# Performance work log

Measured on AMD Instinct MI355X. Metric: run time of the kernel, lower is better.

Reference implementation:

```python
import jax, jax.numpy as jnp
import numpy as np

B, T, D, H = 2, 2048, 1024, 16
DH = D // H
SCALE = DH ** -0.5
NEG_INF = float(np.finfo(np.float32).min)


def setup_inputs() -> dict:
    key = jax.random.key(0)
    ks = jax.random.split(key, 8)
    query = jax.random.normal(ks[0], (B, T, D), dtype=jnp.float32)
    key_t = jax.random.normal(ks[1], (B, T, D), dtype=jnp.float32)
    value = jax.random.normal(ks[2], (B, T, D), dtype=jnp.float32)
    # causal mask: True means blocked (upper triangle)
    mask = ~jnp.tril(jnp.ones((T, T), dtype=bool))
    # key padding: pad tail beyond a random valid length per batch row
    lens = jax.random.randint(ks[3], (B,), T // 2, T)
    key_padding_mask = jnp.arange(T)[None, :] >= lens[:, None]  # [B, T] True = pad
    s = D ** -0.5
    Wq = jax.random.normal(ks[4], (D, D), dtype=jnp.float32) * s
    Wk = jax.random.normal(ks[5], (D, D), dtype=jnp.float32) * s
    Wv = jax.random.normal(ks[6], (D, D), dtype=jnp.float32) * s
    Wo = jax.random.normal(ks[7], (D, D), dtype=jnp.float32) * s
    return {"query": query, "key": key_t, "value": value, "mask": mask,
            "key_padding_mask": key_padding_mask, "Wq": Wq, "Wk": Wk, "Wv": Wv, "Wo": Wo}


def reference(query, key, value, mask, key_padding_mask, Wq, Wk, Wv, Wo):
    # Linear (no bias): y = x @ W.T, then split heads -> [B, H, T, DH]
    def proj(x, W, Tlen):
        return jnp.einsum('btd,ed->bte', x, W).reshape(B, Tlen, H, DH).transpose(0, 2, 1, 3)

    q = proj(query, Wq, T)
    k = proj(key, Wk, T)
    v = proj(value, Wv, T)

    attn = jnp.einsum('bhqd,bhkd->bhqk', q, k) * SCALE  # [B, H, Tq, Tk]
    attn = jnp.where(mask[None, None, :, :], -jnp.inf, attn)
    attn = jnp.where(key_padding_mask[:, None, None, :], -jnp.inf, attn)
    # rows of batches where ALL keys are padding: zero the logits (softmax -> uniform)
    all_masked = jnp.all(key_padding_mask, axis=-1)[:, None, None, None]
    attn = jnp.where(all_masked, 0.0, attn)

    p = jax.nn.softmax(attn, axis=-1)
    p = jnp.where(jnp.isnan(p), 0.0, p)  # scrub NaN rows (all -inf)

    out = jnp.einsum('bhqk,bhkd->bhqd', p, v)
    out = out.transpose(0, 2, 1, 3).reshape(B, T, D)
    return jnp.einsum('btd,ed->bte', out, Wo)
```

## Files before the change

### kernel.cpp

```cpp
#include <hip/hip_runtime.h>

#define B_  2
#define T_  2048
#define D_  1024
#define H_  16
#define DH_ 64
#define M_  4096

typedef _Float16 f16;
typedef _Float16 f16x8 __attribute__((ext_vector_type(8)));
typedef _Float16 f16x4 __attribute__((ext_vector_type(4)));
typedef __fp16   fp16x2 __attribute__((ext_vector_type(2)));
typedef float    f32x4  __attribute__((ext_vector_type(4)));
typedef float    f32x16 __attribute__((ext_vector_type(16)));
typedef unsigned int u32;

__device__ __forceinline__ void async_ld16(const void* g, void* l) {
  __builtin_amdgcn_global_load_lds(
      (const __attribute__((address_space(1))) unsigned int*)g,
      (__attribute__((address_space(3))) unsigned int*)l,
      16, 0, 0);
}

__device__ __forceinline__ u32 pkrtz(float a, float b) {
  union { fp16x2 h; u32 u; } x;
  x.h = __builtin_amdgcn_cvt_pkrtz(a, b);
  return x.u;
}

__global__ __launch_bounds__(256) void convert_all(
    const float* __restrict__ q, const float* __restrict__ k, const float* __restrict__ v,
    const float* __restrict__ wq, const float* __restrict__ wk, const float* __restrict__ wv,
    const float* __restrict__ wo, const void* __restrict__ kpm_raw,
    f16* __restrict__ xh, f16* __restrict__ wh, int* __restrict__ lens_out) {
  int bid = blockIdx.x;
  if (bid >= 8192) {
    int b = bid - 8192;
    __shared__ int s_c8, s_c32;
    if (threadIdx.x == 0) { s_c8 = 0; s_c32 = 0; }
    __syncthreads();
    int tid = threadIdx.x, lane = tid & 63;
    {
      const unsigned char* k8 = (const unsigned char*)kpm_raw + (long)b * T_;
      int cnt = 0;
      for (int j = tid; j < T_; j += 256) cnt += (k8[j] == 0) ? 1 : 0;
#pragma unroll
      for (int off = 1; off < 64; off <<= 1) cnt += __shfl_xor(cnt, off);
      if (lane == 0) atomicAdd(&s_c8, cnt);
    }
    {
      const int* k32 = (const int*)kpm_raw + (long)b * T_;
      int cnt = 0;
      for (int j = tid; j < T_; j += 256) cnt += (k32[j] == 0) ? 1 : 0;
#pragma unroll
      for (int off = 1; off < 64; off <<= 1) cnt += __shfl_xor(cnt, off);
      if (lane == 0) atomicAdd(&s_c32, cnt);
    }
    __syncthreads();
    if (tid == 0) lens_out[b] = (s_c8 == T_) ? s_c32 : s_c8;
    return;
  }
  const float* src;
  f16* dst;
  long base;
  if (bid < 6144) {
    int r = bid >> 11;
    src = (r == 0) ? q : (r == 1) ? k : v;
    dst = xh + (long)r * 4194304;
    base = (long)(bid & 2047) * 2048;
  } else {
    int r = (bid - 6144) >> 9;
    src = (r == 0) ? wq : (r == 1) ? wk : (r == 2) ? wv : wo;
    dst = wh + (long)r * 1048576;
    base = (long)((bid - 6144) & 511) * 2048;
  }
  long e = base + (long)threadIdx.x * 8;
  const float4* s4 = (const float4*)(src + e);
  float4 f0 = s4[0], f1 = s4[1];
  f16x8 o;
  o[0] = (f16)f0.x; o[1] = (f16)f0.y; o[2] = (f16)f0.z; o[3] = (f16)f0.w;
  o[4] = (f16)f1.x; o[5] = (f16)f1.y; o[6] = (f16)f1.z; o[7] = (f16)f1.w;
  *(f16x8*)(dst + e) = o;
}

__global__ __launch_bounds__(256) void gemm_k(
    const f16* __restrict__ Abase, const f16* __restrict__ Wbase,
    f16* __restrict__ Qb, f16* __restrict__ Kb, f16* __restrict__ Vt,
    float* __restrict__ Co, int which) {
  __shared__ __align__(16) f16 As[2][128][32];
  __shared__ __align__(16) f16 Bs[2][128][32];
  const int K = 1024, N = 1024;

  int gx = gridDim.x, gy = gridDim.y;
  int nwg = gx * gy * gridDim.z;
  int bid = blockIdx.x + gx * (blockIdx.y + gy * blockIdx.z);
  int cpx = nwg >> 3;
  int wg = (bid & 7) * cpx + (bid >> 3);
  int bz = wg / (gx * gy);
  int rem = wg - bz * gx * gy;
  int by = rem / gx, bx = rem - by * gx;

  int mode;
  const f16 *A, *W;
  if (which) { mode = 3; A = Abase; W = Wbase; }
  else {
    mode = bz;
    A = Abase + (long)bz * 4194304;
    W = Wbase + (long)bz * 1048576;
  }
  int m0 = by * 128, n0 = bx * 128;
  int tid = threadIdx.x, lane = tid & 63, w = tid >> 6;
  int wm = w >> 1, wn = w & 1;

  int srow = w * 16 + (lane >> 2);
  int scol = (lane & 3) * 8;
  const f16* pa = A + (long)(m0 + srow) * K + scol;
  const f16* pb = W + (long)(n0 + srow) * K + scol;

  f32x4 acc[4][4] = {};
  int row = lane & 15, kq = (lane >> 4) * 8;

  auto STAGE = [&](int k0, int bsel) {
    async_ld16(pa + k0,          &As[bsel][srow][scol]);
    async_ld16(pa + 64 * K + k0, &As[bsel][64 + srow][scol]);
    async_ld16(pb + k0,          &Bs[bsel][srow][scol]);
    async_ld16(pb + 64 * K + k0, &Bs[bsel][64 + srow][scol]);
  };

  STAGE(0, 0);
  asm volatile("s_waitcnt vmcnt(0)" ::: "memory");
  __builtin_amdgcn_s_barrier();

  int cur = 0;
  for (int k0 = 0; k0 < K; k0 += 32) {
    if (k0 + 32 < K) STAGE(k0 + 32, cur ^ 1);
    f16x8 af[4], bfr[4];
#pragma unroll
    for (int m = 0; m < 4; m++) af[m] = *(const f16x8*)&As[cur][wm * 64 + m * 16 + row][kq];
#pragma unroll
    for (int n = 0; n < 4; n++) bfr[n] = *(const f16x8*)&Bs[cur][wn * 64 + n * 16 + row][kq];
#pragma unroll
    for (int m = 0; m < 4; m++)
#pragma unroll
      for (int n = 0; n < 4; n++)
        acc[m][n] = __builtin_amdgcn_mfma_f32_16x16x32_f16(af[m], bfr[n], acc[m][n], 0, 0, 0);
    asm volatile("s_waitcnt vmcnt(0)" ::: "memory");
    __builtin_amdgcn_s_barrier();
    cur ^= 1;
  }

  int r0 = (lane >> 4) * 4;
#pragma unroll
  for (int m = 0; m < 4; m++) {
    int gmb = m0 + wm * 64 + m * 16 + r0;
#pragma unroll
    for (int n = 0; n < 4; n++) {
      int gn = n0 + wn * 64 + n * 16 + row;
      if (mode == 0) {
#pragma unroll
        for (int i = 0; i < 4; i++)
          Qb[(long)(gmb + i) * N + gn] = (f16)(acc[m][n][i] * 0.18033688f);
      } else if (mode == 1) {
#pragma unroll
        for (int i = 0; i < 4; i++)
          Kb[(long)(gmb + i) * N + gn] = (f16)acc[m][n][i];
      } else if (mode == 2) {
        int b = gmb >> 11;
        int t = gmb & 2047;
        int h = gn >> 6, dh = gn & 63;
        f16x4 pk;
#pragma unroll
        for (int i = 0; i < 4; i++) pk[i] = (f16)acc[m][n][i];
        *(f16x4*)&Vt[(long)((b * 16 + h) * 64 + dh) * 2048 + t] = pk;
      } else {
#pragma unroll
        for (int i = 0; i < 4; i++)
          Co[(long)(gmb + i) * N + gn] = acc[m][n][i];
      }
    }
  }
}

__global__ __launch_bounds__(256, 2) void attn_k(
    const f16* __restrict__ Q, const f16* __restrict__ Kp,
    const f16* __restrict__ Vt, const int* __restrict__ Lens,
    f16* __restrict__ Ao) {
  __shared__ __align__(16) f16 Kl[2][4096];
  __shared__ __align__(16) f16 Vl[2][4096];

  int tid = threadIdx.x, lane = tid & 63, w = tid >> 6;
  int bh = blockIdx.x;
  int j  = blockIdx.y;
  int qm = (j < 8) ? (15 - j) : (j - 8);
  int b = bh >> 4, h = bh & 15;
  int r31 = lane & 31, hi = lane >> 5, hi8 = hi * 8;

  int len = Lens[b];
  int q0 = qm * 128;
  int q0w = q0 + w * 32;
  int gq = q0w + r31;

  int blk_kmax = min(q0 + 128, len);
  int wav_kmax = min(q0w + 32, len);
  int NT = (blk_kmax + 63) >> 6;

  const f16* Qh = Q  + (long)b * T_ * D_ + h * 64;
  const f16* Kh = Kp + (long)b * T_ * D_ + h * 64;
  const f16* Vh = Vt + (long)(b * 16 + h) * 64 * T_;

  int srow = w * 16 + (lane >> 3);
  int sc8  = ((lane & 7) ^ ((lane >> 3) & 7)) * 8;
  int ldst = w * 1024 + lane * 8;

  int coff[4];
#pragma unroll
  for (int t = 0; t < 4; t++) coff[t] = ((2 * t + hi) ^ (r31 & 7)) * 8;

  auto STAGE = [&](int t, int bsel) {
    int kb = t * 64;
#pragma unroll
    for (int s = 0; s < 2; s++) {
      int row = srow + s * 8;
      async_ld16(Kh + (long)(kb + row) * D_ + sc8, &Kl[bsel][ldst + s * 512]);
      async_ld16(Vh + (long)row * T_ + kb + sc8,   &Vl[bsel][ldst + s * 512]);
    }
  };

  STAGE(0, 0);
  f16x8 qf[4];
#pragma unroll
  for (int t = 0; t < 4; t++)
    qf[t] = *(const f16x8*)(Qh + (long)gq * D_ + t * 16 + hi8);

  f32x16 o0 = {}, o1 = {};
  float mrun = -1e30f, lrun = 0.f;

  asm volatile("s_waitcnt vmcnt(0)" ::: "memory");
  __syncthreads();

  for (int t = 0; t < NT; t++) {
    int cur = t & 1;
    if (t + 1 < NT) STAGE(t + 1, cur ^ 1);

    int kb = t * 64;
    if (kb < wav_kmax) {
      f32x16 s0 = {}, s1 = {};
#pragma unroll
      for (int tq = 0; tq < 4; tq++) {
        f16x8 k0 = *(const f16x8*)&Kl[cur][(r31)      * 64 + coff[tq]];
        f16x8 k1 = *(const f16x8*)&Kl[cur][(32 + r31) * 64 + coff[tq]];
        s0 = __builtin_amdgcn_mfma_f32_32x32x16_f16(k0, qf[tq], s0, 0, 0, 0);
        s1 = __builtin_amdgcn_mfma_f32_32x32x16_f16(k1, qf[tq], s1, 0, 0, 0);
      }

      bool needmask = (kb + 64 > q0w) || (kb + 64 > len);
      if (needmask) {
#pragma unroll
        for (int r = 0; r < 16; r++) {
          int pat = (r & 3) + 8 * (r >> 2) + 4 * hi;
          int gk0 = kb + pat, gk1 = kb + 32 + pat;
          if (gk0 > gq || gk0 >= len) s0[r] = -1e30f;
          if (gk1 > gq || gk1 >= len) s1[r] = -1e30f;
        }
      }

      float t16[16];
#pragma unroll
      for (int r = 0; r < 16; r++) t16[r] = fmaxf(s0[r], s1[r]);
#pragma unroll
      for (int s = 8; s > 0; s >>= 1)
#pragma unroll
        for (int r = 0; r < s; r++) t16[r] = fmaxf(t16[r], t16[r + s]);
      float mx = fmaxf(t16[0], __shfl_xor(t16[0], 32));

      float mnew = fmaxf(mrun, mx);
      float sf = exp2f(mrun - mnew);
      mrun = mnew;

      float ps[4] = {0.f, 0.f, 0.f, 0.f};
#pragma unroll
      for (int r = 0; r < 16; r++) {
        s0[r] = exp2f(s0[r] - mnew);  ps[r & 3] += s0[r];
        s1[r] = exp2f(s1[r] - mnew);  ps[r & 3] += s1[r];
      }
      float psum = (ps[0] + ps[1]) + (ps[2] + ps[3]);
      lrun = lrun * sf + psum + __shfl_xor(psum, 32);

      o0 *= sf;
      o1 *= sf;

      u32 A0 = pkrtz(s0[0],  s0[1]),  A1 = pkrtz(s0[2],  s0[3]);
      u32 B0 = pkrtz(s0[4],  s0[5]),  B1 = pkrtz(s0[6],  s0[7]);
      u32 C0 = pkrtz(s0[8],  s0[9]),  C1 = pkrtz(s0[10], s0[11]);
      u32 D0 = pkrtz(s0[12], s0[13]), D1 = pkrtz(s0[14], s0[15]);
      u32 E0 = pkrtz(s1[0],  s1[1]),  E1 = pkrtz(s1[2],  s1[3]);
      u32 F0 = pkrtz(s1[4],  s1[5]),  F1 = pkrtz(s1[6],  s1[7]);
      u32 G0 = pkrtz(s1[8],  s1[9]),  G1 = pkrtz(s1[10], s1[11]);
      u32 H0 = pkrtz(s1[12], s1[13]), H1 = pkrtz(s1[14], s1[15]);
      u32 sA0 = __shfl_xor(A0, 32), sA1 = __shfl_xor(A1, 32);
      u32 sB0 = __shfl_xor(B0, 32), sB1 = __shfl_xor(B1, 32);
      u32 sC0 = __shfl_xor(C0, 32), sC1 = __shfl_xor(C1, 32);
      u32 sD0 = __shfl_xor(D0, 32), sD1 = __shfl_xor(D1, 32);
      u32 sE0 = __shfl_xor(E0, 32), sE1 = __shfl_xor(E1, 32);
      u32 sF0 = __shfl_xor(F0, 32), sF1 = __shfl_xor(F1, 32);
      u32 sG0 = __shfl_xor(G0, 32), sG1 = __shfl_xor(G1, 32);
      u32 sH0 = __shfl_xor(H0, 32), sH1 = __shfl_xor(H1, 32);

      union { u32 w[4]; f16x8 v; } f00, f01, f10, f11;
      f00.w[0] = hi ? sB0 : A0;  f00.w[1] = hi ? sB1 : A1;
      f00.w[2] = hi ? B0 : sA0;  f00.w[3] = hi ? B1 : sA1;
      f01.w[0] = hi ? sD0 : C0;  f01.w[1] = hi ? sD1 : C1;
      f01.w[2] = hi ? D0 : sC0;  f01.w[3] = hi ? D1 : sC1;
      f10.w[0] = hi ? sF0 : E0;  f10.w[1] = hi ? sF1 : E1;
      f10.w[2] = hi ? F0 : sE0;  f10.w[3] = hi ? F1 : sE1;
      f11.w[0] = hi ? sH0 : G0;  f11.w[1] = hi ? sH1 : G1;
      f11.w[2] = hi ? H0 : sG0;  f11.w[3] = hi ? H1 : sG1;

      f16x8 v00 = *(const f16x8*)&Vl[cur][(r31)      * 64 + coff[0]];
      f16x8 v01 = *(const f16x8*)&Vl[cur][(r31)      * 64 + coff[1]];
      f16x8 v02 = *(const f16x8*)&Vl[cur][(r31)      * 64 + coff[2]];
      f16x8 v03 = *(const f16x8*)&Vl[cur][(r31)      * 64 + coff[3]];
      f16x8 v10 = *(const f16x8*)&Vl[cur][(32 + r31) * 64 + coff[0]];
      f16x8 v11 = *(const f16x8*)&Vl[cur][(32 + r31) * 64 + coff[1]];
      f16x8 v12 = *(const f16x8*)&Vl[cur][(32 + r31) * 64 + coff[2]];
      f16x8 v13 = *(const f16x8*)&Vl[cur][(32 + r31) * 64 + coff[3]];

      o0 = __builtin_amdgcn_mfma_f32_32x32x16_f16(v00, f00.v, o0, 0, 0, 0);
      o0 = __builtin_amdgcn_mfma_f32_32x32x16_f16(v01, f01.v, o0, 0, 0, 0);
      o0 = __builtin_amdgcn_mfma_f32_32x32x16_f16(v02, f10.v, o0, 0, 0, 0);
      o0 = __builtin_amdgcn_mfma_f32_32x32x16_f16(v03, f11.v, o0, 0, 0, 0);
      o1 = __builtin_amdgcn_mfma_f32_32x32x16_f16(v10, f00.v, o1, 0, 0, 0);
      o1 = __builtin_amdgcn_mfma_f32_32x32x16_f16(v11, f01.v, o1, 0, 0, 0);
      o1 = __builtin_amdgcn_mfma_f32_32x32x16_f16(v12, f10.v, o1, 0, 0, 0);
      o1 = __builtin_amdgcn_mfma_f32_32x32x16_f16(v13, f11.v, o1, 0, 0, 0);
    }

    asm volatile("s_waitcnt vmcnt(0)" ::: "memory");
    __syncthreads();
  }

  float linv = 1.f / lrun;
  f16* Aob = Ao + (long)(b * T_ + gq) * D_ + h * 64 + 4 * hi;
#pragma unroll
  for (int g = 0; g < 4; g++) {
    f16x4 s0, s1;
#pragma unroll
    for (int i = 0; i < 4; i++) {
      s0[i] = (f16)(o0[g * 4 + i] * linv);
      s1[i] = (f16)(o1[g * 4 + i] * linv);
    }
    *(f16x4*)(Aob + 8 * g)      = s0;
    *(f16x4*)(Aob + 32 + 8 * g) = s1;
  }
}

extern "C" void kernel_launch(void* const* d_in, const int* in_sizes, int n_in,
                              void* d_out, int out_size, void* d_ws, size_t ws_size,
                              hipStream_t stream) {
  const float* q  = (const float*)d_in[0];
  const float* k  = (const float*)d_in[1];
  const float* v  = (const float*)d_in[2];
  const void* kpm = d_in[4];
  const float* wq = (const float*)d_in[5];
  const float* wk = (const float*)d_in[6];
  const float* wv = (const float*)d_in[7];
  const float* wo = (const float*)d_in[8];

  char* ws = (char*)d_ws;
  f16* Xh = (f16*)(ws);
  f16* Wh = (f16*)(ws + 25165824);
  f16* Qb = (f16*)(ws + 33554432);
  f16* Kb = (f16*)(ws + 41943040);
  f16* Vt = (f16*)(ws + 50331648);
  f16* Ao = (f16*)(ws + 58720256);
  int* Lens = (int*)d_out;

  convert_all<<<8194, 256, 0, stream>>>(q, k, v, wq, wk, wv, wo, kpm, Xh, Wh, Lens);

  gemm_k<<<dim3(8, 32, 3), 256, 0, stream>>>(Xh, Wh, Qb, Kb, Vt, nullptr, 0);

  attn_k<<<dim3(B_ * H_, T_ / 128), 256, 0, stream>>>(Qb, Kb, Vt, Lens, Ao);

  gemm_k<<<dim3(8, 32, 1), 256, 0, stream>>>(Ao, Wh + 3 * 1048576, nullptr, nullptr,
                                             nullptr, (float*)d_out, 1);
}
```

Measured before the change: 136.6 us.

## Process two 64-key tiles per iteration with quad-buffered LDS and permlane32 swaps

Restructures the attention inner loop to handle 128 keys per iteration across four LDS buffers. This halves the number of barriers and online-softmax rescale steps. The cross-half shuffles plus selects are replaced by v_permlane32_swap instructions. LDS use doubles to 64KB per block, which may limit occupancy under launch_bounds(256,2), and the extra live score registers add register pressure.

```diff
diff --git a/kernel.cpp b/kernel.cpp
--- a/kernel.cpp
+++ b/kernel.cpp
@@ -185,8 +185,8 @@
     const f16* __restrict__ Q, const f16* __restrict__ Kp,
     const f16* __restrict__ Vt, const int* __restrict__ Lens,
     f16* __restrict__ Ao) {
-  __shared__ __align__(16) f16 Kl[2][4096];
-  __shared__ __align__(16) f16 Vl[2][4096];
+  __shared__ __align__(16) f16 Kl[4][4096];
+  __shared__ __align__(16) f16 Vl[4][4096];
 
   int tid = threadIdx.x, lane = tid & 63, w = tid >> 6;
   int bh = blockIdx.x;
@@ -202,7 +202,7 @@
 
   int blk_kmax = min(q0 + 128, len);
   int wav_kmax = min(q0w + 32, len);
-  int NT = (blk_kmax + 63) >> 6;
+  int NR = (blk_kmax + 127) >> 7;
 
   const f16* Qh = Q  + (long)b * T_ * D_ + h * 64;
   const f16* Kh = Kp + (long)b * T_ * D_ + h * 64;
@@ -216,7 +216,7 @@
 #pragma unroll
   for (int t = 0; t < 4; t++) coff[t] = ((2 * t + hi) ^ (r31 & 7)) * 8;
 
-  auto STAGE = [&](int t, int bsel) {
+  auto STAGE64 = [&](int t, int bsel) {
     int kb = t * 64;
 #pragma unroll
     for (int s = 0; s < 2; s++) {
@@ -226,7 +226,8 @@
     }
   };
 
-  STAGE(0, 0);
+  STAGE64(0, 0);
+  STAGE64(1, 1);
   f16x8 qf[4];
 #pragma unroll
   for (int t = 0; t < 4; t++)
@@ -235,42 +236,102 @@
   f32x16 o0 = {}, o1 = {};
   float mrun = -1e30f, lrun = 0.f;
 
+  auto QK = [&](int buf, f32x16& sa, f32x16& sb) {
+#pragma unroll
+    for (int tq = 0; tq < 4; tq++) {
+      f16x8 k0 = *(const f16x8*)&Kl[buf][(r31)      * 64 + coff[tq]];
+      f16x8 k1 = *(const f16x8*)&Kl[buf][(32 + r31) * 64 + coff[tq]];
+      sa = __builtin_amdgcn_mfma_f32_32x32x16_f16(k0, qf[tq], sa, 0, 0, 0);
+      sb = __builtin_amdgcn_mfma_f32_32x32x16_f16(k1, qf[tq], sb, 0, 0, 0);
+    }
+  };
+
+  auto MASK = [&](f32x16& sa, f32x16& sb, int kb) {
+#pragma unroll
+    for (int r = 0; r < 16; r++) {
+      int pat = (r & 3) + 8 * (r >> 2) + 4 * hi;
+      int gk0 = kb + pat, gk1 = kb + 32 + pat;
+      if (gk0 > gq || gk0 >= len) sa[r] = -1e30f;
+      if (gk1 > gq || gk1 >= len) sb[r] = -1e30f;
+    }
+  };
+
+  auto PV = [&](int bufV, f32x16& sa, f32x16& sb) {
+    u32 a0 = pkrtz(sa[0],  sa[1]),  a1 = pkrtz(sa[2],  sa[3]);
+    u32 b0 = pkrtz(sa[4],  sa[5]),  b1 = pkrtz(sa[6],  sa[7]);
+    u32 c0 = pkrtz(sa[8],  sa[9]),  c1 = pkrtz(sa[10], sa[11]);
+    u32 d0 = pkrtz(sa[12], sa[13]), d1 = pkrtz(sa[14], sa[15]);
+    u32 e0 = pkrtz(sb[0],  sb[1]),  e1 = pkrtz(sb[2],  sb[3]);
+    u32 f0_ = pkrtz(sb[4],  sb[5]), f1_ = pkrtz(sb[6],  sb[7]);
+    u32 g0 = pkrtz(sb[8],  sb[9]),  g1 = pkrtz(sb[10], sb[11]);
+    u32 h0 = pkrtz(sb[12], sb[13]), h1 = pkrtz(sb[14], sb[15]);
+    asm("v_permlane32_swap_b32 %0, %1" : "+v"(a0), "+v"(b0));
+    asm("v_permlane32_swap_b32 %0, %1" : "+v"(a1), "+v"(b1));
+    asm("v_permlane32_swap_b32 %0, %1" : "+v"(c0), "+v"(d0));
+    asm("v_permlane32_swap_b32 %0, %1" : "+v"(c1), "+v"(d1));
+    asm("v_permlane32_swap_b32 %0, %1" : "+v"(e0), "+v"(f0_));
+    asm("v_permlane32_swap_b32 %0, %1" : "+v"(e1), "+v"(f1_));
+    asm("v_permlane32_swap_b32 %0, %1" : "+v"(g0), "+v"(h0));
+    asm("v_permlane32_swap_b32 %0, %1" : "+v"(g1), "+v"(h1));
+    union { u32 w[4]; f16x8 v; } f00, f01, f10, f11;
+    f00.w[0] = a0;  f00.w[1] = a1;  f00.w[2] = b0;  f00.w[3] = b1;
+    f01.w[0] = c0;  f01.w[1] = c1;  f01.w[2] = d0;  f01.w[3] = d1;
+    f10.w[0] = e0;  f10.w[1] = e1;  f10.w[2] = f0_; f10.w[3] = f1_;
+    f11.w[0] = g0;  f11.w[1] = g1;  f11.w[2] = h0;  f11.w[3] = h1;
+
+    f16x8 v00 = *(const f16x8*)&Vl[bufV][(r31)      * 64 + coff[0]];
+    f16x8 v01 = *(const f16x8*)&Vl[bufV][(r31)      * 64 + coff[1]];
+    f16x8 v02 = *(const f16x8*)&Vl[bufV][(r31)      * 64 + coff[2]];
+    f16x8 v03 = *(const f16x8*)&Vl[bufV][(r31)      * 64 + coff[3]];
+    f16x8 v10 = *(const f16x8*)&Vl[bufV][(32 + r31) * 64 + coff[0]];
+    f16x8 v11 = *(const f16x8*)&Vl[bufV][(32 + r31) * 64 + coff[1]];
+    f16x8 v12 = *(const f16x8*)&Vl[bufV][(32 + r31) * 64 + coff[2]];
+    f16x8 v13 = *(const f16x8*)&Vl[bufV][(32 + r31) * 64 + coff[3]];
+
+    o0 = __builtin_amdgcn_mfma_f32_32x32x16_f16(v00, f00.v, o0, 0, 0, 0);
+    o0 = __builtin_amdgcn_mfma_f32_32x32x16_f16(v01, f01.v, o0, 0, 0, 0);
+    o0 = __builtin_amdgcn_mfma_f32_32x32x16_f16(v02, f10.v, o0, 0, 0, 0);
+    o0 = __builtin_amdgcn_mfma_f32_32x32x16_f16(v03, f11.v, o0, 0, 0, 0);
+    o1 = __builtin_amdgcn_mfma_f32_32x32x16_f16(v10, f00.v, o1, 0, 0, 0);
+    o1 = __builtin_amdgcn_mfma_f32_32x32x16_f16(v11, f01.v, o1, 0, 0, 0);
+    o1 = __builtin_amdgcn_mfma_f32_32x32x16_f16(v12, f10.v, o1, 0, 0, 0);
+    o1 = __builtin_amdgcn_mfma_f32_32x32x16_f16(v13, f11.v, o1, 0, 0, 0);
+  };
+
   asm volatile("s_waitcnt vmcnt(0)" ::: "memory");
   __syncthreads();
 
-  for (int t = 0; t < NT; t++) {
-    int cur = t & 1;
-    if (t + 1 < NT) STAGE(t + 1, cur ^ 1);
-
-    int kb = t * 64;
+  for (int r = 0; r < NR; r++) {
+    int t0 = 2 * r;
+    int b0buf = t0 & 3, b1buf = (t0 + 1) & 3;
+    if (r + 1 < NR) { STAGE64(t0 + 2, (t0 + 2) & 3); STAGE64(t0 + 3, (t0 + 3) & 3); }
+
+    int kb = r * 128;
     if (kb < wav_kmax) {
-      f32x16 s0 = {}, s1 = {};
-#pragma unroll
-      for (int tq = 0; tq < 4; tq++) {
-        f16x8 k0 = *(const f16x8*)&Kl[cur][(r31)      * 64 + coff[tq]];
-        f16x8 k1 = *(const f16x8*)&Kl[cur][(32 + r31) * 64 + coff[tq]];
-        s0 = __builtin_amdgcn_mfma_f32_32x32x16_f16(k0, qf[tq], s0, 0, 0, 0);
-        s1 = __builtin_amdgcn_mfma_f32_32x32x16_f16(k1, qf[tq], s1, 0, 0, 0);
+      bool has2 = (kb + 64) < wav_kmax;
+      f32x16 s0 = {}, s1 = {}, s2, s3;
+#pragma unroll
+      for (int i = 0; i < 16; i++) { s2[i] = -1e30f; s3[i] = -1e30f; }
+
+      QK(b0buf, s0, s1);
+      if (has2) {
+        f32x16 z0 = {}, z1 = {};
+        QK(b1buf, z0, z1);
+        s2 = z0; s3 = z1;
       }
-
-      bool needmask = (kb + 64 > q0w) || (kb + 64 > len);
-      if (needmask) {
-#pragma unroll
-        for (int r = 0; r < 16; r++) {
-          int pat = (r & 3) + 8 * (r >> 2) + 4 * hi;
-          int gk0 = kb + pat, gk1 = kb + 32 + pat;
-          if (gk0 > gq || gk0 >= len) s0[r] = -1e30f;
-          if (gk1 > gq || gk1 >= len) s1[r] = -1e30f;
-        }
+      if (kb + 128 > q0w || kb + 128 > len) {
+        MASK(s0, s1, kb);
+        if (has2) MASK(s2, s3, kb + 64);
       }
 
       float t16[16];
 #pragma unroll
-      for (int r = 0; r < 16; r++) t16[r] = fmaxf(s0[r], s1[r]);
+      for (int rr = 0; rr < 16; rr++)
+        t16[rr] = fmaxf(fmaxf(s0[rr], s1[rr]), fmaxf(s2[rr], s3[rr]));
 #pragma unroll
       for (int s = 8; s > 0; s >>= 1)
 #pragma unroll
-        for (int r = 0; r < s; r++) t16[r] = fmaxf(t16[r], t16[r + s]);
+        for (int rr = 0; rr < s; rr++) t16[rr] = fmaxf(t16[rr], t16[rr + s]);
       float mx = fmaxf(t16[0], __shfl_xor(t16[0], 32));
 
       float mnew = fmaxf(mrun, mx);
@@ -279,9 +340,16 @@
 
       float ps[4] = {0.f, 0.f, 0.f, 0.f};
 #pragma unroll
-      for (int r = 0; r < 16; r++) {
-        s0[r] = exp2f(s0[r] - mnew);  ps[r & 3] += s0[r];
-        s1[r] = exp2f(s1[r] - mnew);  ps[r & 3] += s1[r];
+      for (int rr = 0; rr < 16; rr++) {
+        s0[rr] = exp2f(s0[rr] - mnew);  ps[rr & 3] += s0[rr];
+        s1[rr] = exp2f(s1[rr] - mnew);  ps[rr & 3] += s1[rr];
+      }
+      if (has2) {
+#pragma unroll
+        for (int rr = 0; rr < 16; rr++) {
+          s2[rr] = exp2f(s2[rr] - mnew);  ps[rr & 3] += s2[rr];
+          s3[rr] = exp2f(s3[rr] - mnew);  ps[rr & 3] += s3[rr];
+        }
       }
       float psum = (ps[0] + ps[1]) + (ps[2] + ps[3]);
       lrun = lrun * sf + psum + __shfl_xor(psum, 32);
@@ -289,50 +357,8 @@
       o0 *= sf;
       o1 *= sf;
 
-      u32 A0 = pkrtz(s0[0],  s0[1]),  A1 = pkrtz(s0[2],  s0[3]);
-      u32 B0 = pkrtz(s0[4],  s0[5]),  B1 = pkrtz(s0[6],  s0[7]);
-      u32 C0 = pkrtz(s0[8],  s0[9]),  C1 = pkrtz(s0[10], s0[11]);
-      u32 D0 = pkrtz(s0[12], s0[13]), D1 = pkrtz(s0[14], s0[15]);
-      u32 E0 = pkrtz(s1[0],  s1[1]),  E1 = pkrtz(s1[2],  s1[3]);
-      u32 F0 = pkrtz(s1[4],  s1[5]),  F1 = pkrtz(s1[6],  s1[7]);
-      u32 G0 = pkrtz(s1[8],  s1[9]),  G1 = pkrtz(s1[10], s1[11]);
-      u32 H0 = pkrtz(s1[12], s1[13]), H1 = pkrtz(s1[14], s1[15]);
-      u32 sA0 = __shfl_xor(A0, 32), sA1 = __shfl_xor(A1, 32);
-      u32 sB0 = __shfl_xor(B0, 32), sB1 = __shfl_xor(B1, 32);
-      u32 sC0 = __shfl_xor(C0, 32), sC1 = __shfl_xor(C1, 32);
-      u32 sD0 = __shfl_xor(D0, 32), sD1 = __shfl_xor(D1, 32);
-      u32 sE0 = __shfl_xor(E0, 32), sE1 = __shfl_xor(E1, 32);
-      u32 sF0 = __shfl_xor(F0, 32), sF1 = __shfl_xor(F1, 32);
-      u32 sG0 = __shfl_xor(G0, 32), sG1 = __shfl_xor(G1, 32);
-      u32 sH0 = __shfl_xor(H0, 32), sH1 = __shfl_xor(H1, 32);
-
-      union { u32 w[4]; f16x8 v; } f00, f01, f10, f11;
-      f00.w[0] = hi ? sB0 : A0;  f00.w[1] = hi ? sB1 : A1;
-      f00.w[2] = hi ? B0 : sA0;  f00.w[3] = hi ? B1 : sA1;
-      f01.w[0] = hi ? sD0 : C0;  f01.w[1] = hi ? sD1 : C1;
-      f01.w[2] = hi ? D0 : sC0;  f01.w[3] = hi ? D1 : sC1;
-      f10.w[0] = hi ? sF0 : E0;  f10.w[1] = hi ? sF1 : E1;
-      f10.w[2] = hi ? F0 : sE0;  f10.w[3] = hi ? F1 : sE1;
-      f11.w[0] = hi ? sH0 : G0;  f11.w[1] = hi ? sH1 : G1;
-      f11.w[2] = hi ? H0 : sG0;  f11.w[3] = hi ? H1 : sG1;
-
-      f16x8 v00 = *(const f16x8*)&Vl[cur][(r31)      * 64 + coff[0]];
-      f16x8 v01 = *(const f16x8*)&Vl[cur][(r31)      * 64 + coff[1]];
-      f16x8 v02 = *(const f16x8*)&Vl[cur][(r31)      * 64 + coff[2]];
-      f16x8 v03 = *(const f16x8*)&Vl[cur][(r31)      * 64 + coff[3]];
-      f16x8 v10 = *(const f16x8*)&Vl[cur][(32 + r31) * 64 + coff[0]];
-      f16x8 v11 = *(const f16x8*)&Vl[cur][(32 + r31) * 64 + coff[1]];
-      f16x8 v12 = *(const f16x8*)&Vl[cur][(32 + r31) * 64 + coff[2]];
-      f16x8 v13 = *(const f16x8*)&Vl[cur][(32 + r31) * 64 + coff[3]];
-
-      o0 = __builtin_amdgcn_mfma_f32_32x32x16_f16(v00, f00.v, o0, 0, 0, 0);
-      o0 = __builtin_amdgcn_mfma_f32_32x32x16_f16(v01, f01.v, o0, 0, 0, 0);
-      o0 = __builtin_amdgcn_mfma_f32_32x32x16_f16(v02, f10.v, o0, 0, 0, 0);
-      o0 = __builtin_amdgcn_mfma_f32_32x32x16_f16(v03, f11.v, o0, 0, 0, 0);
-      o1 = __builtin_amdgcn_mfma_f32_32x32x16_f16(v10, f00.v, o1, 0, 0, 0);
-      o1 = __builtin_amdgcn_mfma_f32_32x32x16_f16(v11, f01.v, o1, 0, 0, 0);
-      o1 = __builtin_amdgcn_mfma_f32_32x32x16_f16(v12, f10.v, o1, 0, 0, 0);
-      o1 = __builtin_amdgcn_mfma_f32_32x32x16_f16(v13, f11.v, o1, 0, 0, 0);
+      PV(b0buf, s0, s1);
+      if (has2) PV(b1buf, s2, s3);
     }
 
     asm volatile("s_waitcnt vmcnt(0)" ::: "memory");
```

After: 127.0 us. 1.08x faster.
